# Kernel optimization log

Measured on AMD Instinct MI355X. Metric: run time of the kernel, lower is better.

Reference implementation:

```python
import jax, jax.numpy as jnp
import numpy as np

N = 50000      # atoms
E = 800000     # edges (avg degree 16)
F = 32         # feature channels
NB = 8         # Bessel basis size
RCUT = 20.0    # Angstrom cutoff (covers the 1nm box)
EV2KJ = 96.4853
NM2A = 10.0


def setup_inputs() -> dict:
    key = jax.random.key(0)
    ks = jax.random.split(key, 12)
    return {
        "positions": jax.random.uniform(ks[0], (N, 3), jnp.float32),      # nm
        "masses": jax.random.uniform(ks[1], (N,), jnp.float32),
        "type_embed": jax.random.normal(ks[2], (3, F), jnp.float32),
        "W_rad1": jax.random.normal(ks[3], (NB, F), jnp.float32) * 0.3,
        "b_rad1": jax.random.normal(ks[4], (F,), jnp.float32) * 0.1,
        "W_rad2": jax.random.normal(ks[5], (F, 2 * F), jnp.float32) * 0.3,
        "W_self": jax.random.normal(ks[6], (F, F), jnp.float32) * 0.3,
        "W_out1": jax.random.normal(ks[7], (2 * F, F), jnp.float32) * 0.3,
        "b_out1": jax.random.normal(ks[8], (F,), jnp.float32) * 0.1,
        "W_out2": jax.random.normal(ks[9], (F, 1), jnp.float32) * 0.3,
        "atom_types": jax.random.randint(ks[10], (N,), 0, 3),
        "edge_index": jax.random.randint(ks[11], (2, E), 0, N),
    }


def reference(positions, masses, type_embed, W_rad1, b_rad1, W_rad2,
              W_self, W_out1, b_out1, W_out2, atom_types, edge_index):
    src, dst = edge_index[0], edge_index[1]

    def energy_eV(pos_A):
        rel = pos_A[dst] - pos_A[src]                       # [E,3] gather
        r = jnp.sqrt(jnp.sum(rel * rel, axis=-1) + 1e-12)   # [E]
        rhat = rel / r[:, None]
        # Bessel radial basis with p=6 polynomial cutoff envelope
        x = r / RCUT
        n = jnp.arange(1, NB + 1, dtype=pos_A.dtype)
        basis = jnp.sin(jnp.pi * n[None, :] * x[:, None]) / r[:, None]  # [E,NB]
        p = 6.0
        env = (1.0 - (p + 1) * (p + 2) / 2 * x**p
               + p * (p + 2) * x**(p + 1)
               - p * (p + 1) / 2 * x**(p + 2))
        env = jnp.where(x < 1.0, env, 0.0)
        rw = jax.nn.silu(basis @ W_rad1 + b_rad1) @ W_rad2   # [E,2F]
        rw = rw * env[:, None]
        w0, w1 = rw[:, :F], rw[:, F:]
        h = type_embed[atom_types]                           # [N,F]
        hs = h[src]                                          # [E,F] gather
        m0 = hs * w0                                         # l=0 messages
        m1 = (hs * w1)[:, :, None] * rhat[:, None, :]        # l=1 messages [E,F,3]
        s = jax.ops.segment_sum(m0, dst, num_segments=N)     # scatter-add
        v = jax.ops.segment_sum(m1.reshape(E, F * 3), dst, num_segments=N)
        v = v.reshape(N, F, 3)
        vnorm = jnp.sqrt(jnp.sum(v * v, axis=-1) + 1e-12)    # invariant [N,F]
        feats = jnp.concatenate([h + s @ W_self, vnorm], axis=1)  # [N,2F]
        per_atom = jax.nn.silu(feats @ W_out1 + b_out1) @ W_out2  # [N,1]
        return jnp.sum(per_atom)

    pos_A = positions * NM2A
    e_eV, g = jax.value_and_grad(energy_eV)(pos_A)
    energy = e_eV * EV2KJ                                    # kJ/mol
    forces = -g * (EV2KJ * NM2A)                             # kJ/mol/nm
    # COM drift correction: mass-weighted net-force subtraction
    net = jnp.sum(forces, axis=0, keepdims=True)
    forces = forces - (masses[:, None] / jnp.sum(masses)) * net
    return energy, forces
```

## Files before the change

### kernel.cpp

```cpp
#include <hip/hip_runtime.h>
#include <math.h>

#define FDIM 32
#define NBASIS 8
#define QP 40
#define DS 18
#define BINW 4096
#define DCAP 4096
#define GSPLIT 8

constexpr float RCUT_C = 20.0f;
constexpr float PI_F = 3.14159265358979323846f;
constexpr float EV2KJ_C = 96.4853f;
constexpr float NM2A_C = 10.0f;

typedef _Float16 f16x8 __attribute__((ext_vector_type(8)));
typedef _Float16 f16x4 __attribute__((ext_vector_type(4)));
typedef float f32x4 __attribute__((ext_vector_type(4)));

__device__ __forceinline__ float sigmoidf_(float z) { return 1.0f / (1.0f + __expf(-z)); }

__device__ __forceinline__ unsigned int pk2_(float a, float b) {
    unsigned short lo = __builtin_bit_cast(unsigned short, (_Float16)a);
    unsigned short hi = __builtin_bit_cast(unsigned short, (_Float16)b);
    return (unsigned int)lo | ((unsigned int)hi << 16);
}
__device__ __forceinline__ float lo16_(unsigned int v) {
    return (float)__builtin_bit_cast(_Float16, (unsigned short)(v & 0xffffu));
}
__device__ __forceinline__ float hi16_(unsigned int v) {
    return (float)__builtin_bit_cast(_Float16, (unsigned short)(v >> 16));
}

__global__ __launch_bounds__(256) void hist_buckets(
    const int* __restrict__ eidx, int* __restrict__ dbcnt, int* __restrict__ sbcnt,
    int E, int dsh, int ssh, int nbd, int nbs)
{
    __shared__ int ld[512];
    __shared__ int ls[64];
    for (int i = threadIdx.x; i < nbd; i += 256) ld[i] = 0;
    for (int i = threadIdx.x; i < nbs; i += 256) ls[i] = 0;
    __syncthreads();
    for (int e = blockIdx.x * 256 + threadIdx.x; e < E; e += gridDim.x * 256) {
        int s = eidx[e];
        int d = eidx[E + e];
        atomicAdd(&ld[d >> dsh], 1);
        atomicAdd(&ls[s >> ssh], 1);
    }
    __syncthreads();
    for (int i = threadIdx.x; i < nbd; i += 256) if (ld[i]) atomicAdd(&dbcnt[i], ld[i]);
    for (int i = threadIdx.x; i < nbs; i += 256) if (ls[i]) atomicAdd(&sbcnt[i], ls[i]);
}

__global__ __launch_bounds__(512) void scan_bases(
    const int* __restrict__ dbcnt, const int* __restrict__ sbcnt,
    int* __restrict__ dbbase, int* __restrict__ sbbase, int nbd, int nbs)
{
    __shared__ int buf[512];
    const int t = threadIdx.x;
    int v = (t < nbd) ? dbcnt[t] : 0;
    buf[t] = v;
    __syncthreads();
    for (int off = 1; off < 512; off <<= 1) {
        int u = (t >= off) ? buf[t - off] : 0;
        __syncthreads();
        buf[t] += u;
        __syncthreads();
    }
    if (t < nbd) dbbase[t] = buf[t] - v;
    if (t == 511) dbbase[nbd] = buf[511];
    __syncthreads();
    int v2 = (t < nbs) ? sbcnt[t] : 0;
    buf[t] = v2;
    __syncthreads();
    for (int off = 1; off < 512; off <<= 1) {
        int u = (t >= off) ? buf[t - off] : 0;
        __syncthreads();
        buf[t] += u;
        __syncthreads();
    }
    if (t < nbs) sbbase[t] = buf[t] - v2;
    if (t == 511) sbbase[nbs] = buf[511];
}

__global__ __launch_bounds__(256) void bin_dst(
    const int* __restrict__ eidx, const int* __restrict__ dbbase,
    int* __restrict__ dbcur, int2* __restrict__ order_sd,
    int E, int dsh, int nbd)
{
    __shared__ int2 rec[BINW];
    __shared__ int lcnt[512], lbase[512], lofs[512];
    const int t = threadIdx.x;
    const int w0 = blockIdx.x * BINW;
    const int n = min(BINW, E - w0);
    if (n <= 0) return;
    for (int i = t; i < nbd; i += 256) lcnt[i] = 0;
    __syncthreads();
    for (int i = t; i < n; i += 256) {
        int e = w0 + i;
        int2 r = make_int2(eidx[e], eidx[E + e]);
        rec[i] = r;
        atomicAdd(&lcnt[r.y >> dsh], 1);
    }
    __syncthreads();
    for (int i = t; i < nbd; i += 256) {
        int c = lcnt[i];
        lbase[i] = c ? atomicAdd(&dbcur[i], c) : 0;
        lofs[i] = 0;
    }
    __syncthreads();
    for (int i = t; i < n; i += 256) {
        int2 r = rec[i];
        int b = r.y >> dsh;
        int pos = lbase[b] + atomicAdd(&lofs[b], 1);
        order_sd[dbbase[b] + pos] = r;
    }
}

__global__ __launch_bounds__(256) void sort_bucket(
    int2* __restrict__ order_sd, const int* __restrict__ dbbase,
    int* __restrict__ sbcur, const int* __restrict__ sbbase,
    int2* __restrict__ srcbin, int dsh, int ssh)
{
    __shared__ int2 rec[DCAP];
    __shared__ int c128[128], o128[128];
    __shared__ int sc[64], sbres[64], so[64];
    const int b = blockIdx.x, t = threadIdx.x;
    const int base = dbbase[b];
    const int cnt = dbbase[b + 1] - base;
    const bool dosort = (dsh <= 7);
    const int kmask = (1 << dsh) - 1;

    for (int start = 0; start < cnt; start += DCAP) {
        const int n = min(DCAP, cnt - start);
        if (t < 128) c128[t] = 0;
        if (t < 64) sc[t] = 0;
        __syncthreads();
        for (int i = t; i < n; i += 256) {
            int2 r = order_sd[base + start + i];
            rec[i] = r;
            if (dosort) atomicAdd(&c128[r.y & kmask], 1);
            atomicAdd(&sc[r.x >> ssh], 1);
        }
        __syncthreads();
        int v0 = (t < 128) ? c128[t] : 0;
        __syncthreads();
        for (int off = 1; off < 128; off <<= 1) {
            int u = (t < 128 && t >= off) ? c128[t - off] : 0;
            __syncthreads();
            if (t < 128) c128[t] += u;
            __syncthreads();
        }
        if (t < 128) o128[t] = c128[t] - v0;
        if (t < 64) {
            int c = sc[t];
            sbres[t] = c ? atomicAdd(&sbcur[t], c) : 0;
            so[t] = 0;
        }
        __syncthreads();
        for (int i = t; i < n; i += 256) {
            int2 r = rec[i];
            int p;
            if (dosort) {
                int pos = atomicAdd(&o128[r.y & kmask], 1);
                p = base + start + pos;
                order_sd[p] = r;
            } else {
                p = base + start + i;
            }
            int sb2 = r.x >> ssh;
            int slot = sbres[sb2] + atomicAdd(&so[sb2], 1);
            srcbin[sbbase[sb2] + slot] = make_int2(r.x, p);
        }
        __syncthreads();
    }
}

__global__ __launch_bounds__(64) void pack_wfrag(
    const float* __restrict__ Wr1, const float* __restrict__ Wr2,
    _Float16* __restrict__ wpack)
{
    const int lane = threadIdx.x;
    const int kb = (lane >> 4) * 8, nb = lane & 15;
    _Float16* o = wpack + (size_t)lane * 64;
    #pragma unroll
    for (int t = 0; t < 2; t++)
        #pragma unroll
        for (int j = 0; j < 8; j++) {
            int k = kb + j;
            o[t * 8 + j] = (k < 8) ? (_Float16)Wr1[k * FDIM + t * 16 + nb] : (_Float16)0.0f;
        }
    #pragma unroll
    for (int t = 0; t < 4; t++)
        #pragma unroll
        for (int j = 0; j < 8; j++)
            o[16 + t * 8 + j] = (_Float16)Wr2[(kb + j) * 64 + t * 16 + nb];
    #pragma unroll
    for (int t = 0; t < 2; t++)
        #pragma unroll
        for (int j = 0; j < 8; j++) {
            int k = kb + j;
            o[48 + t * 8 + j] = (k >= 8 && k < 16) ? (_Float16)Wr1[(k - 8) * FDIM + t * 16 + nb]
                                                   : (_Float16)0.0f;
        }
}

__global__ __launch_bounds__(256) void edge_fwd_mfma(
    const float* __restrict__ pos, const int* __restrict__ types,
    const int2* __restrict__ order_sd,
    const _Float16* __restrict__ wpack, const float* __restrict__ br1,
    const float* __restrict__ temb,
    float* __restrict__ s_acc, float* __restrict__ v_acc, int E)
{
    __shared__ __align__(16) _Float16 sR[4][2560];
    __shared__ float sSt[4][32][4];
    __shared__ int sTy[4][32];
    __shared__ int sKey[4][32];
    __shared__ float sTemb[96];

    const int lane = threadIdx.x & 63;
    const int l32 = threadIdx.x & 31;
    const int hw = (threadIdx.x >> 5) & 1;
    const int w = threadIdx.x >> 6;
    const int gbase = blockIdx.x * 128 + w * 32;

    for (int i = threadIdx.x; i < 96; i += 256) sTemb[i] = temb[i];
    __syncthreads();

    const int kb = (lane >> 4) * 8;
    const f16x8* wp = (const f16x8*)(wpack + (size_t)lane * 64);
    f16x8 bz[2] = { wp[0], wp[1] };
    f16x8 bf[4] = { wp[2], wp[3], wp[4], wp[5] };

    if (lane < 32) {
        const int ed = l32;
        const int p = gbase + ed;
        const bool vld = (p < E);
        int2 sd = vld ? order_sd[p] : make_int2(0, 0);
        float rx = (pos[sd.y * 3 + 0] - pos[sd.x * 3 + 0]) * NM2A_C;
        float ry = (pos[sd.y * 3 + 1] - pos[sd.x * 3 + 1]) * NM2A_C;
        float rz = (pos[sd.y * 3 + 2] - pos[sd.x * 3 + 2]) * NM2A_C;
        float r2 = rx * rx + ry * ry + rz * rz + 1e-12f;
        float r = sqrtf(r2);
        float rinv = 1.0f / r;
        float x = r * (1.0f / RCUT_C);
        float x2 = x * x, x4 = x2 * x2, x6 = x4 * x2, x7 = x6 * x, x8 = x6 * x2;
        float env = (x < 1.0f) ? (1.0f - 28.0f * x6 + 48.0f * x7 - 21.0f * x8) : 0.0f;

        float th = PI_F * x, s1, c1;
        __sincosf(th, &s1, &c1);
        float sp = 0.0f, sn = s1;
        _Float16 av[8];
        #pragma unroll
        for (int n = 0; n < NBASIS; n++) {
            av[n] = (_Float16)(sn * rinv);
            float snx = 2.0f * c1 * sn - sp; sp = sn; sn = snx;
        }
        _Float16* dstA = &sR[w][(ed < 16 ? 0 : 640) + (ed & 15) * QP];
        *(f16x8*)&dstA[0] = *(f16x8*)&av[0];
        *(float4*)&dstA[8]  = make_float4(0.f, 0.f, 0.f, 0.f);
        *(float4*)&dstA[16] = make_float4(0.f, 0.f, 0.f, 0.f);
        *(float4*)&dstA[24] = make_float4(0.f, 0.f, 0.f, 0.f);
        sSt[w][ed][0] = env;
        sSt[w][ed][1] = rx * rinv;
        sSt[w][ed][2] = ry * rinv;
        sSt[w][ed][3] = rz * rinv;
        sTy[w][ed] = types[sd.x];
        sKey[w][ed] = vld ? sd.y : -1;
    }

    {
        const int me = lane & 15;
        f16x8 a1a = *(const f16x8*)&sR[w][me * QP + kb];
        f16x8 a1b = *(const f16x8*)&sR[w][640 + me * QP + kb];
        const f32x4 z4 = {0.f, 0.f, 0.f, 0.f};
        f32x4 Dz0a = __builtin_amdgcn_mfma_f32_16x16x32_f16(a1a, bz[0], z4, 0, 0, 0);
        f32x4 Dz1a = __builtin_amdgcn_mfma_f32_16x16x32_f16(a1a, bz[1], z4, 0, 0, 0);
        f32x4 Dz0b = __builtin_amdgcn_mfma_f32_16x16x32_f16(a1b, bz[0], z4, 0, 0, 0);
        f32x4 Dz1b = __builtin_amdgcn_mfma_f32_16x16x32_f16(a1b, bz[1], z4, 0, 0, 0);
        const int f0 = lane & 15, e0 = (lane >> 4) * 4;
        const float bb0 = br1[f0], bb1 = br1[16 + f0];
        #pragma unroll
        for (int t = 0; t < 2; t++) {
            f32x4 Dza = t ? Dz1a : Dz0a;
            f32x4 Dzb = t ? Dz1b : Dz0b;
            float bb = t ? bb1 : bb0;
            #pragma unroll
            for (int r = 0; r < 4; r++) {
                float za = Dza[r] + bb;
                float zb = Dzb[r] + bb;
                sR[w][1280 + (e0 + r) * QP + t * 16 + f0] = (_Float16)(za * sigmoidf_(za));
                sR[w][1920 + (e0 + r) * QP + t * 16 + f0] = (_Float16)(zb * sigmoidf_(zb));
            }
        }
    }

    {
        const int me = lane & 15;
        f16x8 aqa = *(const f16x8*)&sR[w][1280 + me * QP + kb];
        f16x8 aqb = *(const f16x8*)&sR[w][1920 + me * QP + kb];
        const int cb = lane & 15, e0 = (lane >> 4) * 4;
        float hev[2][2][4];
        #pragma unroll
        for (int tl = 0; tl < 2; tl++)
            #pragma unroll
            for (int fp = 0; fp < 2; fp++)
                #pragma unroll
                for (int r = 0; r < 4; r++) {
                    int ed = tl * 16 + e0 + r;
                    hev[tl][fp][r] = sTemb[sTy[w][ed] * 32 + fp * 16 + cb] * sSt[w][ed][0];
                }
        const f32x4 z4 = {0.f, 0.f, 0.f, 0.f};
        unsigned int* DU = (unsigned int*)&sR[w][0];
        #pragma unroll
        for (int fp = 0; fp < 2; fp++) {
            f32x4 a0 = __builtin_amdgcn_mfma_f32_16x16x32_f16(aqa, bf[fp],     z4, 0, 0, 0);
            f32x4 a1 = __builtin_amdgcn_mfma_f32_16x16x32_f16(aqa, bf[fp + 2], z4, 0, 0, 0);
            f32x4 b0 = __builtin_amdgcn_mfma_f32_16x16x32_f16(aqb, bf[fp],     z4, 0, 0, 0);
            f32x4 b1 = __builtin_amdgcn_mfma_f32_16x16x32_f16(aqb, bf[fp + 2], z4, 0, 0, 0);
            #pragma unroll
            for (int r = 0; r < 4; r++) {
                float ha = hev[0][fp][r], hb = hev[1][fp][r];
                DU[(e0 + r) * 32 + fp * 16 + cb]        = pk2_(a0[r] * ha, a1[r] * ha);
                DU[(16 + e0 + r) * 32 + fp * 16 + cb]   = pk2_(b0[r] * hb, b1[r] * hb);
            }
        }
    }

    const unsigned int* DU = (const unsigned int*)&sR[w][0];
    int runKey = -1;
    float sAcc = 0.f, vXA = 0.f, vYA = 0.f, vZA = 0.f;
    #pragma unroll
    for (int t = 0; t < 2; t++) {
        #pragma unroll
        for (int i = 0; i < 8; i++) {
            const int m = t * 16 + hw * 8 + i;
            const int p = gbase + m;
            if (p >= E) break;
            int k = sKey[w][m];
            if (k != runKey) {
                if (runKey >= 0) {
                    unsafeAtomicAdd(&s_acc[(size_t)runKey * 32 + l32], sAcc);
                    unsafeAtomicAdd(&v_acc[(size_t)runKey * 96 + 0 * 32 + l32], vXA);
                    unsafeAtomicAdd(&v_acc[(size_t)runKey * 96 + 1 * 32 + l32], vYA);
                    unsafeAtomicAdd(&v_acc[(size_t)runKey * 96 + 2 * 32 + l32], vZA);
                }
                runKey = k;
                sAcc = vXA = vYA = vZA = 0.f;
            }
            unsigned int qp = DU[m * 32 + l32];
            float s0 = lo16_(qp);
            float h1 = hi16_(qp);
            sAcc += s0;
            vXA += h1 * sSt[w][m][1];
            vYA += h1 * sSt[w][m][2];
            vZA += h1 * sSt[w][m][3];
        }
    }
    if (runKey >= 0) {
        unsafeAtomicAdd(&s_acc[(size_t)runKey * 32 + l32], sAcc);
        unsafeAtomicAdd(&v_acc[(size_t)runKey * 96 + 0 * 32 + l32], vXA);
        unsafeAtomicAdd(&v_acc[(size_t)runKey * 96 + 1 * 32 + l32], vYA);
        unsafeAtomicAdd(&v_acc[(size_t)runKey * 96 + 2 * 32 + l32], vZA);
    }
}

__global__ __launch_bounds__(64) void atom_mlp(
    const int* __restrict__ types, const float* __restrict__ temb,
    const float* __restrict__ Wself, const float* __restrict__ Wo1,
    const float* __restrict__ bo1, const float* __restrict__ Wo2,
    const float* __restrict__ s_acc, const float* __restrict__ v_acc,
    float* __restrict__ g_all, float* __restrict__ out, int N)
{
    __shared__ __align__(16) float sWs[FDIM * FDIM];
    __shared__ __align__(16) float sWo1[2 * FDIM * FDIM];
    __shared__ __align__(16) float sb[FDIM], sW2o[FDIM], sTE[96];
    const int t = threadIdx.x;
    for (int i = t; i < FDIM * FDIM; i += 64) sWs[i] = Wself[i];
    for (int i = t; i < 2 * FDIM * FDIM; i += 64) sWo1[i] = Wo1[i];
    if (t < FDIM) { sb[t] = bo1[t]; sW2o[t] = Wo2[t]; }
    for (int i = t; i < 96; i += 64) sTE[i] = temb[i];
    __syncthreads();

    int a = blockIdx.x * 64 + t;
    const bool valid = (a < N);
    if (!valid) a = 0;
    const int ty = types[a];

    float u[32];
    {
        float row[32];
        #pragma unroll
        for (int j = 0; j < 32; j++) row[j] = sTE[ty * FDIM + j];
        {
            float s_[32];
            #pragma unroll
            for (int q = 0; q < 8; q++) {
                float4 v = *(const float4*)&s_acc[(size_t)a * FDIM + q * 4];
                s_[q * 4 + 0] = v.x; s_[q * 4 + 1] = v.y;
                s_[q * 4 + 2] = v.z; s_[q * 4 + 3] = v.w;
            }
            #pragma unroll
            for (int k = 0; k < 32; k++) {
                float sk = s_[k];
                #pragma unroll
                for (int q = 0; q < 8; q++) {
                    float4 wv = *(const float4*)&sWs[k * 32 + q * 4];
                    row[q * 4 + 0] += sk * wv.x; row[q * 4 + 1] += sk * wv.y;
                    row[q * 4 + 2] += sk * wv.z; row[q * 4 + 3] += sk * wv.w;
                }
            }
        }
        #pragma unroll
        for (int j = 0; j < 32; j++) u[j] = sb[j];
        #pragma unroll
        for (int k = 0; k < 32; k++) {
            float rk = row[k];
            #pragma unroll
            for (int q = 0; q < 8; q++) {
                float4 w1 = *(const float4*)&sWo1[k * 32 + q * 4];
                u[q * 4 + 0] += rk * w1.x; u[q * 4 + 1] += rk * w1.y;
                u[q * 4 + 2] += rk * w1.z; u[q * 4 + 3] += rk * w1.w;
            }
        }
    }

    float vn[32];
    #pragma unroll
    for (int q = 0; q < 8; q++) {
        float4 x4 = *(const float4*)&v_acc[(size_t)a * 96 +      q * 4];
        float4 y4 = *(const float4*)&v_acc[(size_t)a * 96 + 32 + q * 4];
        float4 z4 = *(const float4*)&v_acc[(size_t)a * 96 + 64 + q * 4];
        vn[q * 4 + 0] = sqrtf(x4.x * x4.x + y4.x * y4.x + z4.x * z4.x + 1e-12f);
        vn[q * 4 + 1] = sqrtf(x4.y * x4.y + y4.y * y4.y + z4.y * z4.y + 1e-12f);
        vn[q * 4 + 2] = sqrtf(x4.z * x4.z + y4.z * y4.z + z4.z * z4.z + 1e-12f);
        vn[q * 4 + 3] = sqrtf(x4.w * x4.w + y4.w * y4.w + z4.w * z4.w + 1e-12f);
    }
    #pragma unroll
    for (int k = 0; k < 32; k++) {
        float vk = vn[k];
        #pragma unroll
        for (int q = 0; q < 8; q++) {
            float4 w2 = *(const float4*)&sWo1[(k + 32) * 32 + q * 4];
            u[q * 4 + 0] += vk * w2.x; u[q * 4 + 1] += vk * w2.y;
            u[q * 4 + 2] += vk * w2.z; u[q * 4 + 3] += vk * w2.w;
        }
    }

    {
        float pa = 0.0f;
        #pragma unroll
        for (int j = 0; j < 32; j++) {
            float z = u[j];
            float sg = sigmoidf_(z);
            pa += z * sg * sW2o[j];
            u[j] = sW2o[j] * (sg * (1.0f + z * (1.0f - sg)));
        }
        if (!valid) pa = 0.0f;
        #pragma unroll
        for (int m = 32; m; m >>= 1) pa += __shfl_xor(pa, m, 64);
        if (t == 0) unsafeAtomicAdd(out, pa * EV2KJ_C);
    }

    float sc[32];
    #pragma unroll
    for (int j = 0; j < 32; j++) {
        float av = 0.f;
        #pragma unroll
        for (int q = 0; q < 8; q++) {
            float4 w2 = *(const float4*)&sWo1[(j + 32) * 32 + q * 4];
            av += u[q * 4 + 0] * w2.x + u[q * 4 + 1] * w2.y
                + u[q * 4 + 2] * w2.z + u[q * 4 + 3] * w2.w;
        }
        sc[j] = av / vn[j];
    }

    float gfr[32];
    #pragma unroll
    for (int j = 0; j < 32; j++) {
        float ar = 0.f;
        #pragma unroll
        for (int q = 0; q < 8; q++) {
            float4 w1 = *(const float4*)&sWo1[j * 32 + q * 4];
            ar += u[q * 4 + 0] * w1.x + u[q * 4 + 1] * w1.y
                + u[q * 4 + 2] * w1.z + u[q * 4 + 3] * w1.w;
        }
        gfr[j] = ar;
    }

    float gs[32];
    #pragma unroll
    for (int j = 0; j < 32; j++) {
        float acc = 0.f;
        #pragma unroll
        for (int q = 0; q < 8; q++) {
            float4 wv = *(const float4*)&sWs[j * 32 + q * 4];
            acc += gfr[q * 4 + 0] * wv.x + gfr[q * 4 + 1] * wv.y
                 + gfr[q * 4 + 2] * wv.z + gfr[q * 4 + 3] * wv.w;
        }
        gs[j] = acc;
    }

    if (valid) {
        #pragma unroll
        for (int q = 0; q < 8; q++) {
            float4 x4 = *(const float4*)&v_acc[(size_t)a * 96 +      q * 4];
            float4 y4 = *(const float4*)&v_acc[(size_t)a * 96 + 32 + q * 4];
            float4 z4 = *(const float4*)&v_acc[(size_t)a * 96 + 64 + q * 4];
            {
                int j = q * 4 + 0;
                *(float4*)&g_all[(size_t)a * 128 + j * 4] =
                    make_float4(gs[j], sc[j] * x4.x, sc[j] * y4.x, sc[j] * z4.x);
            }
            {
                int j = q * 4 + 1;
                *(float4*)&g_all[(size_t)a * 128 + j * 4] =
                    make_float4(gs[j], sc[j] * x4.y, sc[j] * y4.y, sc[j] * z4.y);
            }
            {
                int j = q * 4 + 2;
                *(float4*)&g_all[(size_t)a * 128 + j * 4] =
                    make_float4(gs[j], sc[j] * x4.z, sc[j] * y4.z, sc[j] * z4.z);
            }
            {
                int j = q * 4 + 3;
                *(float4*)&g_all[(size_t)a * 128 + j * 4] =
                    make_float4(gs[j], sc[j] * x4.w, sc[j] * y4.w, sc[j] * z4.w);
            }
        }
    }
}

__global__ __launch_bounds__(256) void edge_bwd_mfma(
    const float* __restrict__ pos, const int* __restrict__ types,
    const int2* __restrict__ order_sd,
    const _Float16* __restrict__ wpack, const float* __restrict__ br1,
    const float* __restrict__ temb,
    const float* __restrict__ g_all,
    float* __restrict__ forces, float4* __restrict__ fbuf, int E)
{
    __shared__ __align__(16) _Float16 sR1[4][1280];
    __shared__ __align__(16) _Float16 sR2[4][1152];
    __shared__ int   sTy[4][16];
    __shared__ float sTemb[96];

    const int lane = threadIdx.x & 63;
    const int l16 = lane & 15;
    const int w = threadIdx.x >> 6;
    const int gbase = blockIdx.x * 64 + w * 16;

    for (int i = threadIdx.x; i < 96; i += 256) sTemb[i] = temb[i];
    __syncthreads();

    const int kb = (lane >> 4) * 8;
    const f16x8* wp = (const f16x8*)(wpack + (size_t)lane * 64);
    f16x8 bz[2] = { wp[0], wp[1] };
    f16x8 bf[4] = { wp[2], wp[3], wp[4], wp[5] };
    f16x8 bt[2] = { wp[6], wp[7] };

    const int p_e = gbase + l16;
    const bool valid = (p_e < E);
    int2 sd = valid ? order_sd[p_e] : make_int2(0, 0);
    const int srcI = sd.x, dstI = sd.y;
    const int key = valid ? sd.y : (-2 - l16);
    (void)srcI;

    float rinv = 1.f, env = 0.f, denv = 0.f, rhx = 0.f, rhy = 0.f, rhz = 0.f;
    if (lane < 16) {
        float rx = (pos[sd.y * 3 + 0] - pos[sd.x * 3 + 0]) * NM2A_C;
        float ry = (pos[sd.y * 3 + 1] - pos[sd.x * 3 + 1]) * NM2A_C;
        float rz = (pos[sd.y * 3 + 2] - pos[sd.x * 3 + 2]) * NM2A_C;
        float r2 = rx * rx + ry * ry + rz * rz + 1e-12f;
        float r = sqrtf(r2);
        rinv = 1.0f / r;
        float x = r * (1.0f / RCUT_C);
        float x2 = x * x, x4 = x2 * x2, x5 = x4 * x, x6 = x4 * x2, x7 = x6 * x, x8 = x6 * x2;
        env = (x < 1.0f) ? (1.0f - 28.0f * x6 + 48.0f * x7 - 21.0f * x8) : 0.0f;
        denv = (x < 1.0f) ? (-168.0f * x5 + 336.0f * x6 - 168.0f * x7) * (1.0f / RCUT_C) : 0.0f;
        rhx = rx * rinv; rhy = ry * rinv; rhz = rz * rinv;

        float th = PI_F * x, s1, c1;
        __sincosf(th, &s1, &c1);
        float sp = 0.0f, sn = s1, cp = 1.0f, cn = c1;
        _Float16 av[16];
        #pragma unroll
        for (int n = 0; n < NBASIS; n++) {
            float basis = sn * rinv;
            float dbdr = (PI_F * (float)(n + 1) * (1.0f / RCUT_C)) * cn * rinv - basis * rinv;
            av[n] = (_Float16)basis;
            av[8 + n] = (_Float16)dbdr;
            float snx = 2.0f * c1 * sn - sp; sp = sn; sn = snx;
            float cnx = 2.0f * c1 * cn - cp; cp = cn; cn = cnx;
        }
        _Float16* dstA = &sR1[w][l16 * QP];
        *(f16x8*)&dstA[0] = *(f16x8*)&av[0];
        *(f16x8*)&dstA[8] = *(f16x8*)&av[8];
        *(float4*)&dstA[16] = make_float4(0.f, 0.f, 0.f, 0.f);
        *(float4*)&dstA[24] = make_float4(0.f, 0.f, 0.f, 0.f);
        sTy[w][l16] = types[sd.x];
    }

    {
        const int me = lane & 15;
        f16x8 a1 = *(const f16x8*)&sR1[w][me * QP + kb];
        const f32x4 z4 = {0.f, 0.f, 0.f, 0.f};
        f32x4 Dz0 = __builtin_amdgcn_mfma_f32_16x16x32_f16(a1, bz[0], z4, 0, 0, 0);
        f32x4 Dz1 = __builtin_amdgcn_mfma_f32_16x16x32_f16(a1, bz[1], z4, 0, 0, 0);
        f32x4 Dt0 = __builtin_amdgcn_mfma_f32_16x16x32_f16(a1, bt[0], z4, 0, 0, 0);
        f32x4 Dt1 = __builtin_amdgcn_mfma_f32_16x16x32_f16(a1, bt[1], z4, 0, 0, 0);
        const int f0 = lane & 15, e0 = (lane >> 4) * 4;
        const float bb0 = br1[f0], bb1 = br1[16 + f0];
        #pragma unroll
        for (int t = 0; t < 2; t++) {
            f32x4 Dz = t ? Dz1 : Dz0;
            f32x4 Dt = t ? Dt1 : Dt0;
            float bb = t ? bb1 : bb0;
            #pragma unroll
            for (int r = 0; r < 4; r++) {
                float z = Dz[r] + bb;
                float sg = sigmoidf_(z);
                sR2[w][(e0 + r) * QP + t * 16 + f0] = (_Float16)(z * sg);
                sR1[w][640 + (e0 + r) * QP + t * 16 + f0] =
                    (_Float16)((sg * (1.0f + z * (1.0f - sg))) * Dt[r]);
            }
        }
    }

    {
        const int me = lane & 15;
        f16x8 aq = *(const f16x8*)&sR2[w][me * QP + kb];
        f16x8 at = *(const f16x8*)&sR1[w][640 + me * QP + kb];
        const int cb = lane & 15, e0 = (lane >> 4) * 4;
        float hsv[2][4];
        #pragma unroll
        for (int r = 0; r < 4; r++) {
            int ty = sTy[w][e0 + r];
            hsv[0][r] = sTemb[ty * 32 + cb];
            hsv[1][r] = sTemb[ty * 32 + 16 + cb];
        }
        const f32x4 z4 = {0.f, 0.f, 0.f, 0.f};
        unsigned int* DqU = (unsigned int*)&sR1[w][0];
        unsigned int* DtU = (unsigned int*)&sR2[w][0];
        #pragma unroll
        for (int fp = 0; fp < 2; fp++) {
            f32x4 q0 = __builtin_amdgcn_mfma_f32_16x16x32_f16(aq, bf[fp],     z4, 0, 0, 0);
            f32x4 q1 = __builtin_amdgcn_mfma_f32_16x16x32_f16(aq, bf[fp + 2], z4, 0, 0, 0);
            f32x4 t0 = __builtin_amdgcn_mfma_f32_16x16x32_f16(at, bf[fp],     z4, 0, 0, 0);
            f32x4 t1 = __builtin_amdgcn_mfma_f32_16x16x32_f16(at, bf[fp + 2], z4, 0, 0, 0);
            unsigned int pq[4], pt[4];
            #pragma unroll
            for (int r = 0; r < 4; r++) {
                float h = hsv[fp][r];
                pq[r] = pk2_(q0[r] * h, q1[r] * h);
                pt[r] = pk2_(t0[r] * h, t1[r] * h);
            }
            const int f = fp * 16 + cb;
            *(uint2*)&DqU[f * DS + e0]     = make_uint2(pq[0], pq[1]);
            *(uint2*)&DqU[f * DS + e0 + 2] = make_uint2(pq[2], pq[3]);
            *(uint2*)&DtU[f * DS + e0]     = make_uint2(pt[0], pt[1]);
            *(uint2*)&DtU[f * DS + e0 + 2] = make_uint2(pt[2], pt[3]);
        }
    }

    {
        const unsigned int* DqU = (const unsigned int*)&sR1[w][0];
        const unsigned int* DtU = (const unsigned int*)&sR2[w][0];
        const int fb = (lane >> 4) * 8;
        const float* gb = g_all + (size_t)dstI * 128;
        float Aa = 0.f, Bb = 0.f, Cc = 0.f, Pp = 0.f;
        float Ap = 0.f, Bp = 0.f, Cp = 0.f, Qq = 0.f;
        #pragma unroll
        for (int ff = 0; ff < 8; ff++) {
            const int f = fb + ff;
            unsigned int qp = DqU[f * DS + l16];
            unsigned int tp = DtU[f * DS + l16];
            float rw0 = lo16_(qp), rw1 = hi16_(qp);
            float u0 = lo16_(tp), u1 = hi16_(tp);
            float4 g4 = *(const float4*)(gb + f * 4);
            Pp += rw0 * g4.x; Qq += u0 * g4.x;
            Aa += rw1 * g4.y; Bb += rw1 * g4.z; Cc += rw1 * g4.w;
            Ap += u1 * g4.y;  Bp += u1 * g4.z;  Cp += u1 * g4.w;
        }
        Pp += __shfl_xor(Pp, 16, 64); Qq += __shfl_xor(Qq, 16, 64);
        Aa += __shfl_xor(Aa, 16, 64); Bb += __shfl_xor(Bb, 16, 64);
        Cc += __shfl_xor(Cc, 16, 64); Ap += __shfl_xor(Ap, 16, 64);
        Bp += __shfl_xor(Bp, 16, 64); Cp += __shfl_xor(Cp, 16, 64);
        Pp += __shfl_xor(Pp, 32, 64); Qq += __shfl_xor(Qq, 32, 64);
        Aa += __shfl_xor(Aa, 32, 64); Bb += __shfl_xor(Bb, 32, 64);
        Cc += __shfl_xor(Cc, 32, 64); Ap += __shfl_xor(Ap, 32, 64);
        Bp += __shfl_xor(Bp, 32, 64); Cp += __shfl_xor(Cp, 32, 64);

        if (lane < 16) {
            float Gx = env * Aa, Gy = env * Bb, Gz = env * Cc;
            float genv = Pp + rhx * Aa + rhy * Bb + rhz * Cc;
            float pc = env * (Qq + rhx * Ap + rhy * Bp + rhz * Cp) + genv * denv;
            float dotg = Gx * rhx + Gy * rhy + Gz * rhz;
            float cx = pc * rhx + (Gx - dotg * rhx) * rinv;
            float cy = pc * rhy + (Gy - dotg * rhy) * rinv;
            float cz = pc * rhz + (Gz - dotg * rhz) * rinv;

            const float SC = EV2KJ_C * NM2A_C;
            if (valid) fbuf[p_e] = make_float4(SC * cx, SC * cy, SC * cz, 0.0f);

            int kk = key;
            #pragma unroll
            for (int d = 1; d < 16; d <<= 1) {
                float ux = __shfl_up(cx, d, 32);
                float uy = __shfl_up(cy, d, 32);
                float uz = __shfl_up(cz, d, 32);
                int uk = __shfl_up(kk, d, 32);
                if (l16 >= d && uk == kk) { cx += ux; cy += uy; cz += uz; }
            }
            int nk = __shfl_down(kk, 1, 32);
            bool leader = (l16 == 15) || (nk != kk);
            if (valid && leader) {
                unsafeAtomicAdd(&forces[(size_t)dstI * 3 + 0], -SC * cx);
                unsafeAtomicAdd(&forces[(size_t)dstI * 3 + 1], -SC * cy);
                unsafeAtomicAdd(&forces[(size_t)dstI * 3 + 2], -SC * cz);
            }
        }
    }
}

__global__ __launch_bounds__(256) void gather_src(
    float* __restrict__ forces, const int* __restrict__ sbbase,
    const int2* __restrict__ srcbin, const float4* __restrict__ fbuf,
    int ssh, int N)
{
    __shared__ float acc[3072];
    const int wg = blockIdx.x;
    const int b = wg / GSPLIT, part = wg % GSPLIT;
    const int base = sbbase[b];
    const int cnt = sbbase[b + 1] - base;
    const int r0 = base + (int)((long long)cnt * part / GSPLIT);
    const int r1 = base + (int)((long long)cnt * (part + 1) / GSPLIT);
    const int abase = b << ssh;
    const bool lok = (ssh <= 10);
    for (int i = threadIdx.x; i < 3072; i += 256) acc[i] = 0.f;
    __syncthreads();
    for (int i = r0 + threadIdx.x; i < r1; i += 256) {
        int2 r = srcbin[i];
        float4 f = fbuf[r.y];
        if (lok) {
            int la = r.x - abase;
            atomicAdd(&acc[la * 3 + 0], f.x);
            atomicAdd(&acc[la * 3 + 1], f.y);
            atomicAdd(&acc[la * 3 + 2], f.z);
        } else {
            unsafeAtomicAdd(&forces[(size_t)r.x * 3 + 0], f.x);
            unsafeAtomicAdd(&forces[(size_t)r.x * 3 + 1], f.y);
            unsafeAtomicAdd(&forces[(size_t)r.x * 3 + 2], f.z);
        }
    }
    __syncthreads();
    if (lok) {
        for (int la = threadIdx.x; la < 1024; la += 256) {
            int a = abase + la;
            if (a < N) {
                float ax = acc[la * 3 + 0], ay = acc[la * 3 + 1], az = acc[la * 3 + 2];
                if (ax != 0.f || ay != 0.f || az != 0.f) {
                    unsafeAtomicAdd(&forces[(size_t)a * 3 + 0], ax);
                    unsafeAtomicAdd(&forces[(size_t)a * 3 + 1], ay);
                    unsafeAtomicAdd(&forces[(size_t)a * 3 + 2], az);
                }
            }
        }
    }
}

__global__ __launch_bounds__(256) void reduce_net(
    const float* __restrict__ f, const float* __restrict__ masses,
    float* __restrict__ accum, int N)
{
    float nx = 0, ny = 0, nz = 0, ms = 0;
    for (int i = blockIdx.x * 256 + threadIdx.x; i < N; i += gridDim.x * 256) {
        nx += f[i * 3 + 0]; ny += f[i * 3 + 1]; nz += f[i * 3 + 2]; ms += masses[i];
    }
    #pragma unroll
    for (int m = 32; m; m >>= 1) {
        nx += __shfl_xor(nx, m, 64);
        ny += __shfl_xor(ny, m, 64);
        nz += __shfl_xor(nz, m, 64);
        ms += __shfl_xor(ms, m, 64);
    }
    __shared__ float red[4][4];
    int w = threadIdx.x >> 6;
    if ((threadIdx.x & 63) == 0) { red[w][0] = nx; red[w][1] = ny; red[w][2] = nz; red[w][3] = ms; }
    __syncthreads();
    if (threadIdx.x == 0) {
        float a0 = 0, a1 = 0, a2 = 0, a3 = 0;
        for (int i = 0; i < 4; i++) { a0 += red[i][0]; a1 += red[i][1]; a2 += red[i][2]; a3 += red[i][3]; }
        unsafeAtomicAdd(accum + 0, a0);
        unsafeAtomicAdd(accum + 1, a1);
        unsafeAtomicAdd(accum + 2, a2);
        unsafeAtomicAdd(accum + 3, a3);
    }
}

__global__ __launch_bounds__(256) void correct_forces(
    float* __restrict__ f, const float* __restrict__ masses,
    const float* __restrict__ accum, int N)
{
    int i = blockIdx.x * 256 + threadIdx.x;
    if (i < N) {
        float c = masses[i] / accum[3];
        f[i * 3 + 0] -= c * accum[0];
        f[i * 3 + 1] -= c * accum[1];
        f[i * 3 + 2] -= c * accum[2];
    }
}

extern "C" void kernel_launch(void* const* d_in, const int* in_sizes, int n_in,
                              void* d_out, int out_size, void* d_ws, size_t ws_size,
                              hipStream_t stream)
{
    (void)n_in; (void)ws_size;
    const float* pos    = (const float*)d_in[0];
    const float* masses = (const float*)d_in[1];
    const float* temb   = (const float*)d_in[2];
    const float* Wr1    = (const float*)d_in[3];
    const float* br1    = (const float*)d_in[4];
    const float* Wr2    = (const float*)d_in[5];
    const float* Wself  = (const float*)d_in[6];
    const float* Wo1    = (const float*)d_in[7];
    const float* bo1    = (const float*)d_in[8];
    const float* Wo2    = (const float*)d_in[9];
    const int* types    = (const int*)d_in[10];
    const int* eidx     = (const int*)d_in[11];
    const int N = in_sizes[1];
    const int E = in_sizes[11] / 2;

    float* out = (float*)d_out;
    float* forces = out + 1;

    int dsh = 7;  while (((N + (1 << dsh) - 1) >> dsh) > 512) dsh++;
    int nbd = (N + (1 << dsh) - 1) >> dsh;
    int ssh = 10; while (((N + (1 << ssh) - 1) >> ssh) > 64) ssh++;
    int nbs = (N + (1 << ssh) - 1) >> ssh;

    float* ws = (float*)d_ws;
    float* s_acc = ws;
    float* v_acc = s_acc + (size_t)N * FDIM;
    float* g_all = v_acc + (size_t)N * 96;
    float* accum = g_all + (size_t)N * 128;
    int* meta = (int*)(accum + 4);
    int* dbcnt  = meta;
    int* sbcnt  = dbcnt + 512;
    int* dbcur  = sbcnt + 64;
    int* sbcur  = dbcur + 512;
    int* dbbase = sbcur + 64;
    int* sbbase = dbbase + 513;
    int2* order_sd = (int2*)(((uintptr_t)(sbbase + 65) + 15) & ~(uintptr_t)15);
    int2* srcbin   = order_sd + E;
    float4* fbuf   = (float4*)(((uintptr_t)(srcbin + E) + 15) & ~(uintptr_t)15);
    _Float16* wpack = (_Float16*)(fbuf + E);

    hipMemsetAsync(d_out, 0, (size_t)out_size * sizeof(float), stream);
    hipMemsetAsync(s_acc, 0, (size_t)N * 128 * sizeof(float), stream);
    hipMemsetAsync(meta, 0, 1152 * sizeof(int), stream);
    hipMemsetAsync(accum, 0, 4 * sizeof(float), stream);

    hist_buckets<<<512, 256, 0, stream>>>(eidx, dbcnt, sbcnt, E, dsh, ssh, nbd, nbs);
    scan_bases<<<1, 512, 0, stream>>>(dbcnt, sbcnt, dbbase, sbbase, nbd, nbs);
    int nBin = (E + BINW - 1) / BINW;
    bin_dst<<<nBin, 256, 0, stream>>>(eidx, dbbase, dbcur, order_sd, E, dsh, nbd);
    sort_bucket<<<nbd, 256, 0, stream>>>(order_sd, dbbase, sbcur, sbbase, srcbin, dsh, ssh);
    pack_wfrag<<<1, 64, 0, stream>>>(Wr1, Wr2, wpack);

    int nAtomBlocks = (N + 63) / 64;
    int nFwdBlocks = (E + 127) / 128;
    int nBwdBlocks = (E + 63) / 64;
    edge_fwd_mfma<<<nFwdBlocks, 256, 0, stream>>>(pos, types, order_sd,
                                                  wpack, br1, temb,
                                                  s_acc, v_acc, E);
    atom_mlp<<<nAtomBlocks, 64, 0, stream>>>(types, temb, Wself, Wo1, bo1, Wo2,
                                             s_acc, v_acc, g_all, out, N);
    edge_bwd_mfma<<<nBwdBlocks, 256, 0, stream>>>(pos, types, order_sd,
                                                  wpack, br1, temb,
                                                  g_all, forces, fbuf, E);
    gather_src<<<nbs * GSPLIT, 256, 0, stream>>>(forces, sbbase, srcbin, fbuf, ssh, N);
    reduce_net<<<64, 256, 0, stream>>>(forces, masses, accum, N);
    correct_forces<<<(N + 255) / 256, 256, 0, stream>>>(forces, masses, accum, N);
}
```

Baseline: 413.1 us.

## Process 32 edges per wavefront in backward edge kernel instead of 16

The backward edge kernel now handles two 16-edge MFMA tiles per wave, so each wave covers 32 edges and the grid is halved. Weight fragments and per-wave setup are reused across twice as many edges. The final per-edge dot product uses 32 lanes with a single cross-half shuffle reduction, and the segmented scan runs over 32 lanes, which gives fewer atomic writes when edges share a destination. In exchange LDS use per block roughly doubles and register pressure rises, which could lower occupancy.

Measured after the change: 399.0 us. 1.04x faster.

```diff
diff --git a/kernel.cpp b/kernel.cpp
--- a/kernel.cpp
+++ b/kernel.cpp
@@ -4,7 +4,7 @@
 #define FDIM 32
 #define NBASIS 8
 #define QP 40
-#define DS 18
+#define DS2 34
 #define BINW 4096
 #define DCAP 4096
 #define GSPLIT 8
@@ -539,15 +539,15 @@
     const float* __restrict__ g_all,
     float* __restrict__ forces, float4* __restrict__ fbuf, int E)
 {
-    __shared__ __align__(16) _Float16 sR1[4][1280];
-    __shared__ __align__(16) _Float16 sR2[4][1152];
-    __shared__ int   sTy[4][16];
+    __shared__ __align__(16) _Float16 sR1[4][2560];
+    __shared__ __align__(16) _Float16 sR2[4][2176];
+    __shared__ int   sTy[4][32];
     __shared__ float sTemb[96];
 
     const int lane = threadIdx.x & 63;
-    const int l16 = lane & 15;
+    const int el = lane & 31;
     const int w = threadIdx.x >> 6;
-    const int gbase = blockIdx.x * 64 + w * 16;
+    const int gbase = blockIdx.x * 128 + w * 32;
 
     for (int i = threadIdx.x; i < 96; i += 256) sTemb[i] = temb[i];
     __syncthreads();
@@ -558,15 +558,14 @@
     f16x8 bf[4] = { wp[2], wp[3], wp[4], wp[5] };
     f16x8 bt[2] = { wp[6], wp[7] };
 
-    const int p_e = gbase + l16;
+    const int p_e = gbase + el;
     const bool valid = (p_e < E);
     int2 sd = valid ? order_sd[p_e] : make_int2(0, 0);
-    const int srcI = sd.x, dstI = sd.y;
-    const int key = valid ? sd.y : (-2 - l16);
-    (void)srcI;
+    const int dstI = sd.y;
+    const int key = valid ? sd.y : (-2 - el);
 
     float rinv = 1.f, env = 0.f, denv = 0.f, rhx = 0.f, rhy = 0.f, rhz = 0.f;
-    if (lane < 16) {
+    if (lane < 32) {
         float rx = (pos[sd.y * 3 + 0] - pos[sd.x * 3 + 0]) * NM2A_C;
         float ry = (pos[sd.y * 3 + 1] - pos[sd.x * 3 + 1]) * NM2A_C;
         float rz = (pos[sd.y * 3 + 2] - pos[sd.x * 3 + 2]) * NM2A_C;
@@ -592,88 +591,114 @@
             float snx = 2.0f * c1 * sn - sp; sp = sn; sn = snx;
             float cnx = 2.0f * c1 * cn - cp; cp = cn; cn = cnx;
         }
-        _Float16* dstA = &sR1[w][l16 * QP];
+        _Float16* dstA = &sR1[w][(el >> 4) * 640 + (el & 15) * QP];
         *(f16x8*)&dstA[0] = *(f16x8*)&av[0];
         *(f16x8*)&dstA[8] = *(f16x8*)&av[8];
         *(float4*)&dstA[16] = make_float4(0.f, 0.f, 0.f, 0.f);
         *(float4*)&dstA[24] = make_float4(0.f, 0.f, 0.f, 0.f);
-        sTy[w][l16] = types[sd.x];
+        sTy[w][el] = types[sd.x];
     }
 
     {
         const int me = lane & 15;
-        f16x8 a1 = *(const f16x8*)&sR1[w][me * QP + kb];
+        f16x8 a1a = *(const f16x8*)&sR1[w][me * QP + kb];
+        f16x8 a1b = *(const f16x8*)&sR1[w][640 + me * QP + kb];
         const f32x4 z4 = {0.f, 0.f, 0.f, 0.f};
-        f32x4 Dz0 = __builtin_amdgcn_mfma_f32_16x16x32_f16(a1, bz[0], z4, 0, 0, 0);
-        f32x4 Dz1 = __builtin_amdgcn_mfma_f32_16x16x32_f16(a1, bz[1], z4, 0, 0, 0);
-        f32x4 Dt0 = __builtin_amdgcn_mfma_f32_16x16x32_f16(a1, bt[0], z4, 0, 0, 0);
-        f32x4 Dt1 = __builtin_amdgcn_mfma_f32_16x16x32_f16(a1, bt[1], z4, 0, 0, 0);
+        f32x4 Dz0a = __builtin_amdgcn_mfma_f32_16x16x32_f16(a1a, bz[0], z4, 0, 0, 0);
+        f32x4 Dz1a = __builtin_amdgcn_mfma_f32_16x16x32_f16(a1a, bz[1], z4, 0, 0, 0);
+        f32x4 Dt0a = __builtin_amdgcn_mfma_f32_16x16x32_f16(a1a, bt[0], z4, 0, 0, 0);
+        f32x4 Dt1a = __builtin_amdgcn_mfma_f32_16x16x32_f16(a1a, bt[1], z4, 0, 0, 0);
+        f32x4 Dz0b = __builtin_amdgcn_mfma_f32_16x16x32_f16(a1b, bz[0], z4, 0, 0, 0);
+        f32x4 Dz1b = __builtin_amdgcn_mfma_f32_16x16x32_f16(a1b, bz[1], z4, 0, 0, 0);
+        f32x4 Dt0b = __builtin_amdgcn_mfma_f32_16x16x32_f16(a1b, bt[0], z4, 0, 0, 0);
+        f32x4 Dt1b = __builtin_amdgcn_mfma_f32_16x16x32_f16(a1b, bt[1], z4, 0, 0, 0);
         const int f0 = lane & 15, e0 = (lane >> 4) * 4;
         const float bb0 = br1[f0], bb1 = br1[16 + f0];
         #pragma unroll
-        for (int t = 0; t < 2; t++) {
-            f32x4 Dz = t ? Dz1 : Dz0;
-            f32x4 Dt = t ? Dt1 : Dt0;
-            float bb = t ? bb1 : bb0;
-            #pragma unroll
-            for (int r = 0; r < 4; r++) {
-                float z = Dz[r] + bb;
-                float sg = sigmoidf_(z);
-                sR2[w][(e0 + r) * QP + t * 16 + f0] = (_Float16)(z * sg);
-                sR1[w][640 + (e0 + r) * QP + t * 16 + f0] =
-                    (_Float16)((sg * (1.0f + z * (1.0f - sg))) * Dt[r]);
+        for (int tl = 0; tl < 2; tl++) {
+            #pragma unroll
+            for (int t = 0; t < 2; t++) {
+                f32x4 Dz = tl ? (t ? Dz1b : Dz0b) : (t ? Dz1a : Dz0a);
+                f32x4 Dt = tl ? (t ? Dt1b : Dt0b) : (t ? Dt1a : Dt0a);
+                float bb = t ? bb1 : bb0;
+                #pragma unroll
+                for (int r = 0; r < 4; r++) {
+                    float z = Dz[r] + bb;
+                    float sg = sigmoidf_(z);
+                    sR2[w][tl * 640 + (e0 + r) * QP + t * 16 + f0] = (_Float16)(z * sg);
+                    sR1[w][1280 + tl * 640 + (e0 + r) * QP + t * 16 + f0] =
+                        (_Float16)((sg * (1.0f + z * (1.0f - sg))) * Dt[r]);
+                }
             }
         }
     }
 
     {
         const int me = lane & 15;
-        f16x8 aq = *(const f16x8*)&sR2[w][me * QP + kb];
-        f16x8 at = *(const f16x8*)&sR1[w][640 + me * QP + kb];
+        f16x8 aqa = *(const f16x8*)&sR2[w][me * QP + kb];
+        f16x8 aqb = *(const f16x8*)&sR2[w][640 + me * QP + kb];
+        f16x8 ata = *(const f16x8*)&sR1[w][1280 + me * QP + kb];
+        f16x8 atb = *(const f16x8*)&sR1[w][1920 + me * QP + kb];
         const int cb = lane & 15, e0 = (lane >> 4) * 4;
-        float hsv[2][4];
-        #pragma unroll
-        for (int r = 0; r < 4; r++) {
-            int ty = sTy[w][e0 + r];
-            hsv[0][r] = sTemb[ty * 32 + cb];
-            hsv[1][r] = sTemb[ty * 32 + 16 + cb];
-        }
+        float hsv[2][2][4];
+        #pragma unroll
+        for (int tl = 0; tl < 2; tl++)
+            #pragma unroll
+            for (int r = 0; r < 4; r++) {
+                int ty = sTy[w][tl * 16 + e0 + r];
+                hsv[tl][0][r] = sTemb[ty * 32 + cb];
+                hsv[tl][1][r] = sTemb[ty * 32 + 16 + cb];
+            }
         const f32x4 z4 = {0.f, 0.f, 0.f, 0.f};
         unsigned int* DqU = (unsigned int*)&sR1[w][0];
         unsigned int* DtU = (unsigned int*)&sR2[w][0];
         #pragma unroll
         for (int fp = 0; fp < 2; fp++) {
-            f32x4 q0 = __builtin_amdgcn_mfma_f32_16x16x32_f16(aq, bf[fp],     z4, 0, 0, 0);
-            f32x4 q1 = __builtin_amdgcn_mfma_f32_16x16x32_f16(aq, bf[fp + 2], z4, 0, 0, 0);
-            f32x4 t0 = __builtin_amdgcn_mfma_f32_16x16x32_f16(at, bf[fp],     z4, 0, 0, 0);
-            f32x4 t1 = __builtin_amdgcn_mfma_f32_16x16x32_f16(at, bf[fp + 2], z4, 0, 0, 0);
+            f32x4 q0a = __builtin_amdgcn_mfma_f32_16x16x32_f16(aqa, bf[fp],     z4, 0, 0, 0);
+            f32x4 q1a = __builtin_amdgcn_mfma_f32_16x16x32_f16(aqa, bf[fp + 2], z4, 0, 0, 0);
+            f32x4 q0b = __builtin_amdgcn_mfma_f32_16x16x32_f16(aqb, bf[fp],     z4, 0, 0, 0);
+            f32x4 q1b = __builtin_amdgcn_mfma_f32_16x16x32_f16(aqb, bf[fp + 2], z4, 0, 0, 0);
+            f32x4 t0a = __builtin_amdgcn_mfma_f32_16x16x32_f16(ata, bf[fp],     z4, 0, 0, 0);
+            f32x4 t1a = __builtin_amdgcn_mfma_f32_16x16x32_f16(ata, bf[fp + 2], z4, 0, 0, 0);
+            f32x4 t0b = __builtin_amdgcn_mfma_f32_16x16x32_f16(atb, bf[fp],     z4, 0, 0, 0);
+            f32x4 t1b = __builtin_amdgcn_mfma_f32_16x16x32_f16(atb, bf[fp + 2], z4, 0, 0, 0);
+            const int f = fp * 16 + cb;
             unsigned int pq[4], pt[4];
             #pragma unroll
             for (int r = 0; r < 4; r++) {
-                float h = hsv[fp][r];
-                pq[r] = pk2_(q0[r] * h, q1[r] * h);
-                pt[r] = pk2_(t0[r] * h, t1[r] * h);
-            }
-            const int f = fp * 16 + cb;
-            *(uint2*)&DqU[f * DS + e0]     = make_uint2(pq[0], pq[1]);
-            *(uint2*)&DqU[f * DS + e0 + 2] = make_uint2(pq[2], pq[3]);
-            *(uint2*)&DtU[f * DS + e0]     = make_uint2(pt[0], pt[1]);
-            *(uint2*)&DtU[f * DS + e0 + 2] = make_uint2(pt[2], pt[3]);
+                float h = hsv[0][fp][r];
+                pq[r] = pk2_(q0a[r] * h, q1a[r] * h);
+                pt[r] = pk2_(t0a[r] * h, t1a[r] * h);
+            }
+            *(uint2*)&DqU[f * DS2 + e0]     = make_uint2(pq[0], pq[1]);
+            *(uint2*)&DqU[f * DS2 + e0 + 2] = make_uint2(pq[2], pq[3]);
+            *(uint2*)&DtU[f * DS2 + e0]     = make_uint2(pt[0], pt[1]);
+            *(uint2*)&DtU[f * DS2 + e0 + 2] = make_uint2(pt[2], pt[3]);
+            #pragma unroll
+            for (int r = 0; r < 4; r++) {
+                float h = hsv[1][fp][r];
+                pq[r] = pk2_(q0b[r] * h, q1b[r] * h);
+                pt[r] = pk2_(t0b[r] * h, t1b[r] * h);
+            }
+            *(uint2*)&DqU[f * DS2 + 16 + e0]     = make_uint2(pq[0], pq[1]);
+            *(uint2*)&DqU[f * DS2 + 16 + e0 + 2] = make_uint2(pq[2], pq[3]);
+            *(uint2*)&DtU[f * DS2 + 16 + e0]     = make_uint2(pt[0], pt[1]);
+            *(uint2*)&DtU[f * DS2 + 16 + e0 + 2] = make_uint2(pt[2], pt[3]);
         }
     }
 
     {
         const unsigned int* DqU = (const unsigned int*)&sR1[w][0];
         const unsigned int* DtU = (const unsigned int*)&sR2[w][0];
-        const int fb = (lane >> 4) * 8;
+        const int fg = lane >> 5;
         const float* gb = g_all + (size_t)dstI * 128;
         float Aa = 0.f, Bb = 0.f, Cc = 0.f, Pp = 0.f;
         float Ap = 0.f, Bp = 0.f, Cp = 0.f, Qq = 0.f;
         #pragma unroll
-        for (int ff = 0; ff < 8; ff++) {
-            const int f = fb + ff;
-            unsigned int qp = DqU[f * DS + l16];
-            unsigned int tp = DtU[f * DS + l16];
+        for (int ff = 0; ff < 16; ff++) {
+            const int f = fg * 16 + ff;
+            unsigned int qp = DqU[f * DS2 + el];
+            unsigned int tp = DtU[f * DS2 + el];
             float rw0 = lo16_(qp), rw1 = hi16_(qp);
             float u0 = lo16_(tp), u1 = hi16_(tp);
             float4 g4 = *(const float4*)(gb + f * 4);
@@ -681,16 +706,12 @@
             Aa += rw1 * g4.y; Bb += rw1 * g4.z; Cc += rw1 * g4.w;
             Ap += u1 * g4.y;  Bp += u1 * g4.z;  Cp += u1 * g4.w;
         }
-        Pp += __shfl_xor(Pp, 16, 64); Qq += __shfl_xor(Qq, 16, 64);
-        Aa += __shfl_xor(Aa, 16, 64); Bb += __shfl_xor(Bb, 16, 64);
-        Cc += __shfl_xor(Cc, 16, 64); Ap += __shfl_xor(Ap, 16, 64);
-        Bp += __shfl_xor(Bp, 16, 64); Cp += __shfl_xor(Cp, 16, 64);
         Pp += __shfl_xor(Pp, 32, 64); Qq += __shfl_xor(Qq, 32, 64);
         Aa += __shfl_xor(Aa, 32, 64); Bb += __shfl_xor(Bb, 32, 64);
         Cc += __shfl_xor(Cc, 32, 64); Ap += __shfl_xor(Ap, 32, 64);
         Bp += __shfl_xor(Bp, 32, 64); Cp += __shfl_xor(Cp, 32, 64);
 
-        if (lane < 16) {
+        if (lane < 32) {
             float Gx = env * Aa, Gy = env * Bb, Gz = env * Cc;
             float genv = Pp + rhx * Aa + rhy * Bb + rhz * Cc;
             float pc = env * (Qq + rhx * Ap + rhy * Bp + rhz * Cp) + genv * denv;
@@ -704,15 +725,15 @@
 
             int kk = key;
             #pragma unroll
-            for (int d = 1; d < 16; d <<= 1) {
+            for (int d = 1; d < 32; d <<= 1) {
                 float ux = __shfl_up(cx, d, 32);
                 float uy = __shfl_up(cy, d, 32);
                 float uz = __shfl_up(cz, d, 32);
                 int uk = __shfl_up(kk, d, 32);
-                if (l16 >= d && uk == kk) { cx += ux; cy += uy; cz += uz; }
+                if (el >= d && uk == kk) { cx += ux; cy += uy; cz += uz; }
             }
             int nk = __shfl_down(kk, 1, 32);
-            bool leader = (l16 == 15) || (nk != kk);
+            bool leader = (el == 31) || (nk != kk);
             if (valid && leader) {
                 unsafeAtomicAdd(&forces[(size_t)dstI * 3 + 0], -SC * cx);
                 unsafeAtomicAdd(&forces[(size_t)dstI * 3 + 1], -SC * cy);
@@ -869,7 +890,7 @@
 
     int nAtomBlocks = (N + 63) / 64;
     int nFwdBlocks = (E + 127) / 128;
-    int nBwdBlocks = (E + 63) / 64;
+    int nBwdBlocks = (E + 127) / 128;
     edge_fwd_mfma<<<nFwdBlocks, 256, 0, stream>>>(pos, types, order_sd,
                                                   wpack, br1, temb,
                                                   s_acc, v_acc, E);
```
